# Performance work log

Measured on AMD Instinct MI355X. Metric: run time of the kernel, lower is better.

The kernel has to match this reference:

```python
import jax, jax.numpy as jnp
import numpy as np

B, S, D, H = 2, 2048, 1024, 16
HD = D // H  # 64
NEG = 1.0e9


def setup_inputs() -> dict:
    key = jax.random.key(0)
    ks = jax.random.split(key, 9)
    scale = 1.0 / np.sqrt(D)
    return {
        "q_in": jax.random.normal(ks[0], (B, S, D), jnp.float32),
        "k_in": jax.random.normal(ks[1], (B, S, D), jnp.float32),
        "v_in": jax.random.normal(ks[2], (B, S, D), jnp.float32),
        "Wq": jax.random.normal(ks[3], (D, D), jnp.float32) * scale,
        "bq": jnp.zeros((D,), jnp.float32),
        "Wk": jax.random.normal(ks[4], (D, D), jnp.float32) * scale,
        "bk": jnp.zeros((D,), jnp.float32),
        "Wv": jax.random.normal(ks[5], (D, D), jnp.float32) * scale,
        "bv": jnp.zeros((D,), jnp.float32),
        "Wo": jax.random.normal(ks[6], (D, D), jnp.float32) * scale,
        "bo": jnp.zeros((D,), jnp.float32),
    }


def _split_heads(x):
    # [B,S,D] -> [B,H,S,HD]
    return x.reshape(B, S, H, HD).transpose(0, 2, 1, 3)


def reference(q_in, k_in, v_in, Wq, bq, Wk, bk, Wv, bv, Wo, bo):
    q = _split_heads(q_in @ Wq + bq)
    k = _split_heads(k_in @ Wk + bk)
    v = _split_heads(v_in @ Wv + bv)
    # scaled dot-product attention with additive causal mask (use_causal_mask=True)
    scores = jnp.einsum("bhqd,bhkd->bhqk", q, k) / jnp.sqrt(jnp.float32(HD))
    causal = jnp.tril(jnp.ones((S, S), jnp.float32))  # band_part(ones, -1, 0)
    scores = scores + (causal - 1.0) * NEG
    weights = jax.nn.softmax(scores, axis=-1)
    attn = jnp.einsum("bhqk,bhkd->bhqd", weights, v)
    concat = attn.transpose(0, 2, 1, 3).reshape(B, S, D)
    return concat @ Wo + bo
```

## Files before the change

kernel.cpp:

```cpp
#include <hip/hip_runtime.h>

#define B_  2
#define S_  2048
#define D_  1024
#define H_  16
#define HD_ 64
#define MM  (B_ * S_)

typedef __bf16 bf16;
typedef __attribute__((ext_vector_type(8))) __bf16 bf16x8;
typedef __attribute__((ext_vector_type(4))) __bf16 bf16x4;
typedef __attribute__((ext_vector_type(4))) float  f32x4;

__device__ inline float exp2g(float x) { return __builtin_amdgcn_exp2f(x); }

__device__ inline bf16x8 load8(const bf16* p) { return *(const bf16x8*)p; }
__device__ inline bf16x8 load8(const float* p) {
  float4 a = *(const float4*)p;
  float4 b = *(const float4*)(p + 4);
  bf16x8 r;
  r[0] = (bf16)a.x; r[1] = (bf16)a.y; r[2] = (bf16)a.z; r[3] = (bf16)a.w;
  r[4] = (bf16)b.x; r[5] = (bf16)b.y; r[6] = (bf16)b.z; r[7] = (bf16)b.w;
  return r;
}

__device__ inline void gld16(void* lds, const void* g) {
  __builtin_amdgcn_global_load_lds(
      (const __attribute__((address_space(1))) unsigned int*)g,
      (__attribute__((address_space(3))) unsigned int*)lds, 16, 0, 0);
}

__global__ __launch_bounds__(256) void transpose_w(
    const float* __restrict__ W0, const float* __restrict__ W1,
    const float* __restrict__ W2, const float* __restrict__ W3,
    bf16* __restrict__ T0, bf16* __restrict__ T1,
    bf16* __restrict__ T2, bf16* __restrict__ T3,
    const float* __restrict__ X0, const float* __restrict__ X1,
    const float* __restrict__ X2,
    bf16* __restrict__ Y0, bf16* __restrict__ Y1, bf16* __restrict__ Y2) {
  const int z = blockIdx.z;
  if (z >= 4) {
    const int p = z - 4, t = p >> 2;
    const float* src = t == 0 ? X0 : t == 1 ? X1 : X2;
    bf16* dst = t == 0 ? Y0 : t == 1 ? Y1 : Y2;
    long base = ((long)(p & 3) << 20) +
                (long)(blockIdx.y * 32 + blockIdx.x) * 1024 + threadIdx.x * 4;
    float4 v = *(const float4*)&src[base];
    bf16x4 o4;
    o4[0] = (bf16)v.x; o4[1] = (bf16)v.y; o4[2] = (bf16)v.z; o4[3] = (bf16)v.w;
    *(bf16x4*)&dst[base] = o4;
    return;
  }
  __shared__ bf16 t[32][40];
  const float* in = z == 0 ? W0 : z == 1 ? W1 : z == 2 ? W2 : W3;
  bf16* out = z == 0 ? T0 : z == 1 ? T1 : z == 2 ? T2 : T3;
  const int tx = threadIdx.x & 31;
  const int ty = threadIdx.x >> 5;
  const int r0 = blockIdx.y * 32, c0 = blockIdx.x * 32;
#pragma unroll
  for (int j = 0; j < 32; j += 8)
    t[ty + j][tx] = (bf16)in[(long)(r0 + ty + j) * D_ + (c0 + tx)];
  __syncthreads();
#pragma unroll
  for (int j = 0; j < 32; j += 8)
    out[(long)(c0 + ty + j) * D_ + (r0 + tx)] = t[tx][ty + j];
}

__global__ __launch_bounds__(256) void transpose_v64(const bf16* __restrict__ V,
                                                     bf16* __restrict__ VT) {
  __shared__ bf16 t[64][72];
  const int tid = threadIdx.x;
  const int s0 = blockIdx.x * 64;
  const int bh = blockIdx.y;
  const int b = bh >> 4, h = bh & 15;
  const bf16* ip = V + (long)b * S_ * D_ + h * HD_;
  bf16* op = VT + (long)bh * HD_ * S_;
#pragma unroll
  for (int i = 0; i < 2; ++i) {
    int c = tid + i * 256;
    int r = c >> 3, cc = (c & 7) * 8;
    *(bf16x8*)&t[r][cc] = *(const bf16x8*)&ip[(long)(s0 + r) * D_ + cc];
  }
  __syncthreads();
#pragma unroll
  for (int i = 0; i < 2; ++i) {
    int c = tid + i * 256;
    int d = c >> 3, sc = (c & 7) * 8;
    bf16x8 v;
#pragma unroll
    for (int j = 0; j < 8; ++j) v[j] = t[sc + j][d];
    *(bf16x8*)&op[(long)d * S_ + s0 + sc] = v;
  }
}

template <typename AT, typename OT>
__global__ __launch_bounds__(256) void gemm_bt_dma(
    const AT* __restrict__ A0, const AT* __restrict__ A1, const AT* __restrict__ A2,
    const bf16* __restrict__ B0, const bf16* __restrict__ B1, const bf16* __restrict__ B2,
    const float* __restrict__ c0, const float* __restrict__ c1, const float* __restrict__ c2,
    OT* __restrict__ C0, OT* __restrict__ C1, OT* __restrict__ C2,
    int M, int N, int K) {
  __shared__ bf16 lA[2][128][32];
  __shared__ bf16 lB[2][128][32];
  const int z = blockIdx.z;
  const AT*    A    = z == 0 ? A0 : z == 1 ? A1 : A2;
  const bf16*  Bt   = z == 0 ? B0 : z == 1 ? B1 : B2;
  const float* bias = z == 0 ? c0 : z == 1 ? c1 : c2;
  OT*          C    = z == 0 ? C0 : z == 1 ? C1 : C2;

  const int tid = threadIdx.x;
  const int lane = tid & 63, wave = tid >> 6;
  const int quad = lane >> 4, l16 = lane & 15;
  const int id = blockIdx.x + (blockIdx.y << 3);
  const int nid = (id & 7) * 32 + (id >> 3);
  const int bm = (nid >> 3) * 128, bn = (nid & 7) * 128;
  const int wm = (wave >> 1) * 64, wn = (wave & 1) * 64;

  f32x4 acc[4][4] = {};

  for (int k0 = 0; k0 < K; k0 += 64) {
    __syncthreads();
#pragma unroll
    for (int hh = 0; hh < 2; ++hh) {
#pragma unroll
      for (int i = 0; i < 2; ++i) {
        const int nbase = wave * 128 + i * 64;
        const int n = nbase + lane;
        const int row = n >> 2, kc = (n & 3) * 8;
        gld16(&lB[hh][0][0] + (long)nbase * 8,
              &Bt[(long)(bn + row) * K + k0 + hh * 32 + kc]);
        if constexpr (__is_same(AT, bf16))
          gld16(&lA[hh][0][0] + (long)nbase * 8,
                &A[(long)(bm + row) * K + k0 + hh * 32 + kc]);
      }
      if constexpr (!__is_same(AT, bf16)) {
#pragma unroll
        for (int i = 0; i < 2; ++i) {
          int c = tid + i * 256;
          int row = c >> 2, kc = (c & 3) * 8;
          *(bf16x8*)&lA[hh][row][kc] =
              load8(&A[(long)(bm + row) * K + k0 + hh * 32 + kc]);
        }
      }
    }
    __syncthreads();
#pragma unroll
    for (int hh = 0; hh < 2; ++hh) {
      bf16x8 af[4], bfr[4];
#pragma unroll
      for (int i = 0; i < 4; ++i) {
        af[i]  = *(const bf16x8*)&lA[hh][wm + i * 16 + l16][quad * 8];
        bfr[i] = *(const bf16x8*)&lB[hh][wn + i * 16 + l16][quad * 8];
      }
#pragma unroll
      for (int mi = 0; mi < 4; ++mi)
#pragma unroll
        for (int ni = 0; ni < 4; ++ni)
          acc[mi][ni] = __builtin_amdgcn_mfma_f32_16x16x32_bf16(
              af[mi], bfr[ni], acc[mi][ni], 0, 0, 0);
    }
  }

#pragma unroll
  for (int mi = 0; mi < 4; ++mi)
#pragma unroll
    for (int ni = 0; ni < 4; ++ni) {
      int col = bn + wn + ni * 16 + l16;
      float bv = bias[col];
#pragma unroll
      for (int r = 0; r < 4; ++r) {
        int row = bm + wm + mi * 16 + quad * 4 + r;
        C[(long)row * N + col] = (OT)(acc[mi][ni][r] + bv);
      }
    }
}

__global__ __launch_bounds__(256) void gemm_bt_64(const bf16* __restrict__ A,
                                                  const bf16* __restrict__ Bt,
                                                  const float* __restrict__ bias,
                                                  float* __restrict__ C,
                                                  int M, int N, int K) {
  __shared__ bf16 lA[2][128][32];
  __shared__ bf16 lB[2][64][32];
  const int tid = threadIdx.x;
  const int lane = tid & 63, wave = tid >> 6;
  const int quad = lane >> 4, l16 = lane & 15;
  const int id = blockIdx.x + (blockIdx.y << 4);
  const int nid = (id & 7) * 64 + (id >> 3);
  const int bm = (nid >> 4) * 128, bn = (nid & 15) * 64;
  const int wm = (wave >> 1) * 64, wn = (wave & 1) * 32;

  f32x4 acc[4][2] = {};

  for (int k0 = 0; k0 < K; k0 += 64) {
    __syncthreads();
#pragma unroll
    for (int hh = 0; hh < 2; ++hh) {
#pragma unroll
      for (int i = 0; i < 2; ++i) {
        const int nbase = wave * 128 + i * 64;
        const int n = nbase + lane;
        const int row = n >> 2, kc = (n & 3) * 8;
        gld16(&lA[hh][0][0] + (long)nbase * 8,
              &A[(long)(bm + row) * K + k0 + hh * 32 + kc]);
      }
      {
        const int nbase = wave * 64;
        const int n = nbase + lane;
        const int row = n >> 2, kc = (n & 3) * 8;
        gld16(&lB[hh][0][0] + (long)nbase * 8,
              &Bt[(long)(bn + row) * K + k0 + hh * 32 + kc]);
      }
    }
    __syncthreads();
#pragma unroll
    for (int hh = 0; hh < 2; ++hh) {
      bf16x8 af[4], bfr[2];
#pragma unroll
      for (int i = 0; i < 4; ++i)
        af[i] = *(const bf16x8*)&lA[hh][wm + i * 16 + l16][quad * 8];
#pragma unroll
      for (int i = 0; i < 2; ++i)
        bfr[i] = *(const bf16x8*)&lB[hh][wn + i * 16 + l16][quad * 8];
#pragma unroll
      for (int mi = 0; mi < 4; ++mi)
#pragma unroll
        for (int ni = 0; ni < 2; ++ni)
          acc[mi][ni] = __builtin_amdgcn_mfma_f32_16x16x32_bf16(
              af[mi], bfr[ni], acc[mi][ni], 0, 0, 0);
    }
  }

#pragma unroll
  for (int mi = 0; mi < 4; ++mi)
#pragma unroll
    for (int ni = 0; ni < 2; ++ni) {
      int col = bn + wn + ni * 16 + l16;
      float bv = bias[col];
#pragma unroll
      for (int r = 0; r < 4; ++r) {
        int row = bm + wm + mi * 16 + quad * 4 + r;
        C[(long)row * N + col] = acc[mi][ni][r] + bv;
      }
    }
}

#define SCALE_LOG2E 0.1803368801111244f

__device__ inline void attn_step5(bool diag, int qloc, int quad, int l16,
                                  const bf16 (*lKb)[64], const bf16 (*lVb)[64],
                                  bf16 (*lpw)[72], const bf16x8* aq,
                                  f32x4* o, float& l_s) {
  const int sw = l16 & 7;
  f32x4 s[4];
#pragma unroll
  for (int ni = 0; ni < 4; ++ni) {
    f32x4 a = {};
#pragma unroll
    for (int c = 0; c < 2; ++c) {
      bf16x8 kf = *(const bf16x8*)&lKb[ni * 16 + l16][((c * 4 + quad) ^ sw) * 8];
      a = __builtin_amdgcn_mfma_f32_16x16x32_bf16(kf, aq[c], a, 0, 0, 0);
    }
    s[ni] = a * SCALE_LOG2E;
  }
  if (diag) {
#pragma unroll
    for (int ni = 0; ni < 4; ++ni)
#pragma unroll
      for (int r = 0; r < 4; ++r)
        if (ni * 16 + quad * 4 + r > qloc) s[ni][r] = -1e9f;
  }
  float rs = 0.f;
#pragma unroll
  for (int ni = 0; ni < 4; ++ni) {
    bf16x4 p4;
#pragma unroll
    for (int r = 0; r < 4; ++r) {
      float p = exp2g(s[ni][r]);
      p4[r] = (bf16)p;
      rs += p;
    }
    *(bf16x4*)&lpw[l16][ni * 16 + quad * 4] = p4;
  }
  l_s += rs;
#pragma unroll
  for (int c = 0; c < 2; ++c) {
    bf16x8 ap = *(const bf16x8*)&lpw[l16][c * 32 + quad * 8];
#pragma unroll
    for (int di = 0; di < 4; ++di) {
      bf16x8 vf = *(const bf16x8*)&lVb[di * 16 + l16][((c * 4 + quad) ^ sw) * 8];
      o[di] = __builtin_amdgcn_mfma_f32_16x16x32_bf16(vf, ap, o[di], 0, 0, 0);
    }
  }
}

__device__ inline void store_o(bf16* Ob, int qrow, int lane, int quad, int l16,
                               bf16 (*lpw)[72], const f32x4* o, float l_s) {
  float rs = l_s;
  rs += __shfl_xor(rs, 16);
  rs += __shfl_xor(rs, 32);
  const float inv = 1.0f / rs;
#pragma unroll
  for (int di = 0; di < 4; ++di) {
    bf16x4 p4;
#pragma unroll
    for (int r = 0; r < 4; ++r) p4[r] = (bf16)(o[di][r] * inv);
    *(bf16x4*)&lpw[l16][di * 16 + quad * 4] = p4;
  }
  const int q = lane >> 2, db = (lane & 3) * 16;
  bf16x8 v0 = *(const bf16x8*)&lpw[q][db];
  bf16x8 v1 = *(const bf16x8*)&lpw[q][db + 8];
  *(bf16x8*)&Ob[(long)(qrow + q) * D_ + db] = v0;
  *(bf16x8*)&Ob[(long)(qrow + q) * D_ + db + 8] = v1;
}

__global__ __launch_bounds__(512) void flash_attn7(const bf16* __restrict__ Q,
                                                   const bf16* __restrict__ K,
                                                   const bf16* __restrict__ VT,
                                                   bf16* __restrict__ O) {
  __shared__ bf16 lK[2][64][64];
  __shared__ bf16 lV[2][64][64];
  __shared__ bf16 lp[8][16][72];
  const int tid = threadIdx.x;
  const int lane = tid & 63, wave = tid >> 6;
  const int quad = lane >> 4, l16 = lane & 15;
  const int x = blockIdx.x, bh = blockIdx.y;
  const bool flip = (bh & 16) != 0;
  const int qtA = flip ? 30 - 2 * x : 2 * x;
  const int qtB = qtA + 1;
  const bool isB = wave >= 4;
  const int w4 = wave & 3;
  const int myqt = isB ? qtB : qtA;
  const int b = bh >> 4, h = bh & 15;
  const bf16* Qb = Q + (long)b * S_ * D_ + h * HD_;
  const bf16* Kb = K + (long)b * S_ * D_ + h * HD_;
  const bf16* Vb = VT + (long)bh * HD_ * S_;
  const int qrow = myqt * 64 + w4 * 16;
  const int qloc = w4 * 16 + l16;

  bf16x8 aq[2];
#pragma unroll
  for (int c = 0; c < 2; ++c)
    aq[c] = *(const bf16x8*)&Qb[(long)(qrow + l16) * D_ + c * 32 + quad * 8];

  f32x4 o[4] = {};
  float l_s = 0.f;

  const int srow = tid >> 3, scol = tid & 7;
  const int swcol = (scol ^ (srow & 7)) * 8;

  bf16x8 kreg, vreg;
  kreg = *(const bf16x8*)&Kb[(long)srow * D_ + scol * 8];
  vreg = *(const bf16x8*)&Vb[(long)srow * S_ + scol * 8];
  *(bf16x8*)&lK[0][srow][swcol] = kreg;
  *(bf16x8*)&lV[0][srow][swcol] = vreg;
  __syncthreads();

  const int ktMax = qtB;
  for (int kt = 0; kt <= ktMax; ++kt) {
    const int p = kt & 1;
    if (kt < ktMax) {
      const long k0 = (long)(kt + 1) * 64;
      kreg = *(const bf16x8*)&Kb[(k0 + srow) * D_ + scol * 8];
      vreg = *(const bf16x8*)&Vb[(long)srow * S_ + k0 + scol * 8];
    }
    if (isB || kt <= qtA)
      attn_step5(kt == myqt, qloc, quad, l16, lK[p], lV[p], lp[wave], aq,
                 o, l_s);
    if (kt < ktMax) {
      *(bf16x8*)&lK[1 - p][srow][swcol] = kreg;
      *(bf16x8*)&lV[1 - p][srow][swcol] = vreg;
      __syncthreads();
    }
  }

  bf16* Ob = O + (long)b * S_ * D_ + h * HD_;
  store_o(Ob, qrow, lane, quad, l16, lp[wave], o, l_s);
}

extern "C" void kernel_launch(void* const* d_in, const int* in_sizes, int n_in,
                              void* d_out, int out_size, void* d_ws, size_t ws_size,
                              hipStream_t stream) {
  (void)in_sizes; (void)n_in; (void)out_size;
  const float* q_in = (const float*)d_in[0];
  const float* k_in = (const float*)d_in[1];
  const float* v_in = (const float*)d_in[2];
  const float* Wq   = (const float*)d_in[3];
  const float* bq   = (const float*)d_in[4];
  const float* Wk   = (const float*)d_in[5];
  const float* bk   = (const float*)d_in[6];
  const float* Wv   = (const float*)d_in[7];
  const float* bv   = (const float*)d_in[8];
  const float* Wo   = (const float*)d_in[9];
  const float* bo   = (const float*)d_in[10];
  float* out = (float*)d_out;

  bf16* ws = (bf16*)d_ws;
  const size_t WSZ = (size_t)D_ * D_;
  const size_t TSZ = (size_t)B_ * S_ * D_;
  bf16* WqT = ws;
  bf16* WkT = WqT + WSZ;
  bf16* WvT = WkT + WSZ;
  bf16* WoT = WvT + WSZ;
  bf16* Qp  = WoT + WSZ;
  bf16* Kp  = Qp + TSZ;
  bf16* Vp  = Kp + TSZ;
  bf16* VTp = Vp + TSZ;
  bf16* Ap  = VTp + TSZ;
  bf16* Xq  = VTp;
  bf16* Xk  = Ap;
  bf16* Xv  = Ap + TSZ;
  const bool pre = ws_size >= (4 * WSZ + 6 * TSZ) * sizeof(bf16);

  dim3 blk(256);
  transpose_w<<<dim3(32, 32, pre ? 16 : 4), blk, 0, stream>>>(
      Wq, Wk, Wv, Wo, WqT, WkT, WvT, WoT, q_in, k_in, v_in, Xq, Xk, Xv);

  if (pre)
    gemm_bt_dma<bf16, bf16><<<dim3(8, 32, 3), blk, 0, stream>>>(
        Xq, Xk, Xv, WqT, WkT, WvT, bq, bk, bv, Qp, Kp, Vp, MM, D_, D_);
  else
    gemm_bt_dma<float, bf16><<<dim3(8, 32, 3), blk, 0, stream>>>(
        q_in, k_in, v_in, WqT, WkT, WvT, bq, bk, bv, Qp, Kp, Vp, MM, D_, D_);

  transpose_v64<<<dim3(S_ / 64, B_ * H_), blk, 0, stream>>>(Vp, VTp);

  flash_attn7<<<dim3(16, B_ * H_), dim3(512), 0, stream>>>(Qp, Kp, VTp, Ap);

  gemm_bt_64<<<dim3(16, 32), blk, 0, stream>>>(Ap, WoT, bo, out, MM, D_, D_);
}
```

Baseline: 214.9 us.

## Deepen K/V prefetch to two tiles ahead in flash attention loop

Unrolls the flash attention key loop by two and keeps two register sets of K/V tiles, so the global loads for a tile are issued two steps before it is written to shared memory. The aim is to hide more global load latency behind the attention math. In exchange it uses more registers, which may lower occupancy at 512 threads. The number of key tiles is always even here, which the unrolled loop relies on.

Result: faster. 205.3 us (-4.5%).

```diff
diff --git a/kernel.cpp b/kernel.cpp
--- a/kernel.cpp
+++ b/kernel.cpp
@@ -314,7 +314,7 @@
   *(bf16x8*)&Ob[(long)(qrow + q) * D_ + db + 8] = v1;
 }
 
-__global__ __launch_bounds__(512) void flash_attn7(const bf16* __restrict__ Q,
+__global__ __launch_bounds__(512) void flash_attn8(const bf16* __restrict__ Q,
                                                    const bf16* __restrict__ K,
                                                    const bf16* __restrict__ VT,
                                                    bf16* __restrict__ O) {
@@ -348,28 +348,40 @@
 
   const int srow = tid >> 3, scol = tid & 7;
   const int swcol = (scol ^ (srow & 7)) * 8;
-
-  bf16x8 kreg, vreg;
-  kreg = *(const bf16x8*)&Kb[(long)srow * D_ + scol * 8];
-  vreg = *(const bf16x8*)&Vb[(long)srow * S_ + scol * 8];
-  *(bf16x8*)&lK[0][srow][swcol] = kreg;
-  *(bf16x8*)&lV[0][srow][swcol] = vreg;
+  const int ktMax = qtB;
+
+  bf16x8 rkA, rvA, rkB, rvB;
+  rkA = *(const bf16x8*)&Kb[(long)srow * D_ + scol * 8];
+  rvA = *(const bf16x8*)&Vb[(long)srow * S_ + scol * 8];
+  *(bf16x8*)&lK[0][srow][swcol] = rkA;
+  *(bf16x8*)&lV[0][srow][swcol] = rvA;
+  rkA = *(const bf16x8*)&Kb[(long)(64 + srow) * D_ + scol * 8];
+  rvA = *(const bf16x8*)&Vb[(long)srow * S_ + 64 + scol * 8];
   __syncthreads();
 
-  const int ktMax = qtB;
-  for (int kt = 0; kt <= ktMax; ++kt) {
-    const int p = kt & 1;
-    if (kt < ktMax) {
-      const long k0 = (long)(kt + 1) * 64;
-      kreg = *(const bf16x8*)&Kb[(k0 + srow) * D_ + scol * 8];
-      vreg = *(const bf16x8*)&Vb[(long)srow * S_ + k0 + scol * 8];
+  for (int kt = 0; kt < ktMax; kt += 2) {
+    if (kt + 2 <= ktMax) {
+      const long k0 = (long)(kt + 2) * 64;
+      rkB = *(const bf16x8*)&Kb[(k0 + srow) * D_ + scol * 8];
+      rvB = *(const bf16x8*)&Vb[(long)srow * S_ + k0 + scol * 8];
     }
     if (isB || kt <= qtA)
-      attn_step5(kt == myqt, qloc, quad, l16, lK[p], lV[p], lp[wave], aq,
+      attn_step5(kt == myqt, qloc, quad, l16, lK[0], lV[0], lp[wave], aq,
                  o, l_s);
-    if (kt < ktMax) {
-      *(bf16x8*)&lK[1 - p][srow][swcol] = kreg;
-      *(bf16x8*)&lV[1 - p][srow][swcol] = vreg;
+    *(bf16x8*)&lK[1][srow][swcol] = rkA;
+    *(bf16x8*)&lV[1][srow][swcol] = rvA;
+    __syncthreads();
+    if (kt + 3 <= ktMax) {
+      const long k0 = (long)(kt + 3) * 64;
+      rkA = *(const bf16x8*)&Kb[(k0 + srow) * D_ + scol * 8];
+      rvA = *(const bf16x8*)&Vb[(long)srow * S_ + k0 + scol * 8];
+    }
+    if (isB || kt + 1 <= qtA)
+      attn_step5(kt + 1 == myqt, qloc, quad, l16, lK[1], lV[1], lp[wave], aq,
+                 o, l_s);
+    if (kt + 1 < ktMax) {
+      *(bf16x8*)&lK[0][srow][swcol] = rkB;
+      *(bf16x8*)&lV[0][srow][swcol] = rvB;
       __syncthreads();
     }
   }
@@ -425,7 +437,7 @@
 
   transpose_v64<<<dim3(S_ / 64, B_ * H_), blk, 0, stream>>>(Vp, VTp);
 
-  flash_attn7<<<dim3(16, B_ * H_), dim3(512), 0, stream>>>(Qp, Kp, VTp, Ap);
+  flash_attn8<<<dim3(16, B_ * H_), dim3(512), 0, stream>>>(Qp, Kp, VTp, Ap);
 
   gemm_bt_64<<<dim3(16, 32), blk, 0, stream>>>(Ap, WoT, bo, out, MM, D_, D_);
 }
```
